# Optimization experiments

Hardware: AMD Instinct MI355X
Metric: run time of the kernel (lower is better)

The kernel has to match this reference:

```python
import jax, jax.numpy as jnp
import numpy as np
import math

B, T, C, H, L, V = 8, 511, 1024, 16, 8, 128  # T = block_size - 1
D = C // H
FF = 4 * C


def setup_inputs() -> dict:
    key = jax.random.key(0)
    ks = jax.random.split(key, 12)
    std = 0.02
    n = lambda k, s: (jax.random.normal(k, s, dtype=jnp.float32) * std)
    idx = jax.random.randint(ks[0], (B, T), 0, V)
    idx = jnp.where(idx == 2, 3, idx)  # avoid pad token so logits[idx!=2] keeps all rows
    return {
        "idx": idx,
        "tok_emb": n(ks[1], (V, C)),
        "pos_emb": n(ks[2], (T, C)),
        "ln1_w": jnp.ones((L, C)), "ln1_b": jnp.zeros((L, C)),
        "Wq": n(ks[3], (L, C, C)), "bq": jnp.zeros((L, C)),
        "Wk": n(ks[4], (L, C, C)), "bk": jnp.zeros((L, C)),
        "Wv": n(ks[5], (L, C, C)), "bv": jnp.zeros((L, C)),
        "Wp": n(ks[6], (L, C, C)), "bp": jnp.zeros((L, C)),
        "ln2_w": jnp.ones((L, C)), "ln2_b": jnp.zeros((L, C)),
        "W1": n(ks[7], (L, C, FF)), "b1": jnp.zeros((L, FF)),
        "W2": n(ks[8], (L, FF, C)), "b2": jnp.zeros((L, C)),
        "lnf_w": jnp.ones((C,)), "lnf_b": jnp.zeros((C,)),
        "head_w": n(ks[9], (V, C)),
    }


def _ln(x, w, b):
    m = x.mean(-1, keepdims=True)
    v = ((x - m) ** 2).mean(-1, keepdims=True)
    return (x - m) * jax.lax.rsqrt(v + 1e-5) * w + b


def reference(idx, tok_emb, pos_emb, ln1_w, ln1_b, Wq, bq, Wk, bk, Wv, bv, Wp, bp,
              ln2_w, ln2_b, W1, b1, W2, b2, lnf_w, lnf_b, head_w):
    x = tok_emb[idx] + pos_emb[None, :, :]                      # [B,T,C]
    mask = jnp.tril(jnp.ones((T, T), dtype=bool))
    scale = 1.0 / math.sqrt(D)

    def block(x, p):
        h = _ln(x, p["ln1_w"], p["ln1_b"])
        q = (h @ p["Wq"] + p["bq"]).reshape(B, T, H, D).transpose(0, 2, 1, 3)
        k = (h @ p["Wk"] + p["bk"]).reshape(B, T, H, D).transpose(0, 2, 1, 3)
        v = (h @ p["Wv"] + p["bv"]).reshape(B, T, H, D).transpose(0, 2, 1, 3)
        att = jnp.einsum('bhqd,bhkd->bhqk', q, k) * scale       # [B,H,T,T]
        att = jnp.where(mask, att, -jnp.inf)
        att = jax.nn.softmax(att, axis=-1)
        y = jnp.einsum('bhqk,bhkd->bhqd', att, v)
        y = y.transpose(0, 2, 1, 3).reshape(B, T, C)
        x = x + y @ p["Wp"] + p["bp"]
        h = _ln(x, p["ln2_w"], p["ln2_b"])
        h = jax.nn.gelu(h @ p["W1"] + p["b1"], approximate=False)
        x = x + h @ p["W2"] + p["b2"]
        return x, None

    stacked = dict(ln1_w=ln1_w, ln1_b=ln1_b, Wq=Wq, bq=bq, Wk=Wk, bk=bk, Wv=Wv, bv=bv,
                   Wp=Wp, bp=bp, ln2_w=ln2_w, ln2_b=ln2_b, W1=W1, b1=b1, W2=W2, b2=b2)
    x, _ = jax.lax.scan(block, x, stacked)
    x = _ln(x, lnf_w, lnf_b)
    logits = x @ head_w.T                                       # [B,T,V]
    # logits[idx != 2] with no 2-tokens present == all rows flattened
    return logits.reshape(B * T, V)
```

## Files before the change

### kernel.cpp

```cpp
#include <hip/hip_runtime.h>
#include <hip/hip_bf16.h>

typedef unsigned short u16;
typedef unsigned int   u32;
typedef __attribute__((ext_vector_type(8))) __bf16 bf16x8;
typedef __attribute__((ext_vector_type(4))) float  f32x4;

static constexpr int NB  = 8;
static constexpr int TT  = 511;
static constexpr int CC  = 1024;
static constexpr int HH  = 16;
static constexpr int LL  = 8;
static constexpr int VV  = 128;
static constexpr int FF_ = 4096;
static constexpr int MV  = NB * TT;
static constexpr int MP  = 4096;
static constexpr int TP  = 512;

#define DEVI static __device__ __forceinline__

DEVI u16 f2bf(float f) {
  u32 u = __builtin_bit_cast(u32, f);
  u = (u + 0x7fffu + ((u >> 16) & 1u)) >> 16;
  return (u16)u;
}

DEVI void gload16(const void* g, void* lds) {
  auto gp = (const __attribute__((address_space(1))) u32*)(uintptr_t)g;
  auto lp = (__attribute__((address_space(3))) u32*)(uintptr_t)lds;
  __builtin_amdgcn_global_load_lds(gp, lp, 16, 0, 0);
}

__global__ __launch_bounds__(256) void k_transpose(const float* __restrict__ in,
                                                   u16* __restrict__ out, int K, int N,
                                                   size_t is, size_t os) {
  in  += (size_t)blockIdx.z * is;
  out += (size_t)blockIdx.z * os;
  __shared__ u16 tile[64][66];
  int nb = blockIdx.x * 64, kb = blockIdx.y * 64;
  int t = threadIdx.x;
  int r = t >> 4, c4 = (t & 15) * 4;
#pragma unroll
  for (int i = 0; i < 4; ++i) {
    int k = r + i * 16;
    float4 v = *(const float4*)(in + (size_t)(kb + k) * N + nb + c4);
    tile[k][c4 + 0] = f2bf(v.x); tile[k][c4 + 1] = f2bf(v.y);
    tile[k][c4 + 2] = f2bf(v.z); tile[k][c4 + 3] = f2bf(v.w);
  }
  __syncthreads();
#pragma unroll
  for (int i = 0; i < 4; ++i) {
    int n = r + i * 16;
    ushort4 o;
    o.x = tile[c4 + 0][n]; o.y = tile[c4 + 1][n];
    o.z = tile[c4 + 2][n]; o.w = tile[c4 + 3][n];
    *(ushort4*)(out + (size_t)(nb + n) * K + kb + c4) = o;
  }
}

__global__ __launch_bounds__(256) void k_cast_bf16(const float* __restrict__ in,
                                                   u16* __restrict__ out, int n) {
  int i = blockIdx.x * 256 + threadIdx.x;
  if (i < n) out[i] = f2bf(in[i]);
}

__global__ __launch_bounds__(256) void k_pack_qkv_bias(const float* __restrict__ bq,
                                                       const float* __restrict__ bk,
                                                       const float* __restrict__ bv,
                                                       float* __restrict__ out) {
  int i = blockIdx.x * 256 + threadIdx.x;
  int l = i / (3 * CC), c = i % (3 * CC);
  float v = (c < CC) ? bq[l * CC + c] : (c < 2 * CC) ? bk[l * CC + c - CC] : bv[l * CC + c - 2 * CC];
  out[i] = v;
}

__global__ __launch_bounds__(256) void k_embed(const int* __restrict__ idx,
                                               const float* __restrict__ tok,
                                               const float* __restrict__ pos,
                                               float* __restrict__ x) {
  int row = blockIdx.x;
  int c4 = threadIdx.x * 4;
  if (row >= MV) {
    *(float4*)(x + (size_t)row * CC + c4) = make_float4(0.f, 0.f, 0.f, 0.f);
    return;
  }
  int t = row % TT;
  int tid = idx[row];
  float4 a = *(const float4*)(tok + (size_t)tid * CC + c4);
  float4 p = *(const float4*)(pos + (size_t)t * CC + c4);
  a.x += p.x; a.y += p.y; a.z += p.z; a.w += p.w;
  *(float4*)(x + (size_t)row * CC + c4) = a;
}

__global__ __launch_bounds__(256) void k_ln(const float* __restrict__ x,
                                            const float* __restrict__ w,
                                            const float* __restrict__ b,
                                            u16* __restrict__ out) {
  int wid = threadIdx.x >> 6, l = threadIdx.x & 63;
  int row = blockIdx.x * 4 + wid;
  const float* xr = x + (size_t)row * CC;
  float4 v[4];
  float s = 0.f, sq = 0.f;
#pragma unroll
  for (int i = 0; i < 4; ++i) {
    v[i] = *(const float4*)(xr + (i * 64 + l) * 4);
    s  += v[i].x + v[i].y + v[i].z + v[i].w;
    sq += v[i].x * v[i].x + v[i].y * v[i].y + v[i].z * v[i].z + v[i].w * v[i].w;
  }
#pragma unroll
  for (int o = 32; o; o >>= 1) { s += __shfl_xor(s, o); sq += __shfl_xor(sq, o); }
  float mean = s * (1.f / CC);
  float var  = sq * (1.f / CC) - mean * mean;
  float rs = rsqrtf(var + 1e-5f);
#pragma unroll
  for (int i = 0; i < 4; ++i) {
    int c = (i * 64 + l) * 4;
    float4 wv = *(const float4*)(w + c);
    float4 bv = *(const float4*)(b + c);
    ushort4 o4;
    o4.x = f2bf((v[i].x - mean) * rs * wv.x + bv.x);
    o4.y = f2bf((v[i].y - mean) * rs * wv.y + bv.y);
    o4.z = f2bf((v[i].z - mean) * rs * wv.z + bv.z);
    o4.w = f2bf((v[i].w - mean) * rs * wv.w + bv.w);
    *(ushort4*)(out + (size_t)row * CC + c) = o4;
  }
}

template <int BN, int EPI, int KSPLIT>
__global__ __launch_bounds__(512, 2) void k_gemm2(const u16* __restrict__ A,
                                                  const u16* __restrict__ Wt,
                                                  const float* __restrict__ bias,
                                                  float* __restrict__ outf,
                                                  u16* __restrict__ outb,
                                                  int N, int K, int gridN, int Mv) {
  constexpr int WN  = BN / 64;
  constexpr int GLB = BN / 64;
  constexpr int GL  = 4 + GLB;
  constexpr int ATILE = 256 * 64;
  __shared__ u16 lds[2][ATILE + BN * 64];

  int t = threadIdx.x, l = t & 63, wid = t >> 6;
  int wr = wid >> 2, wc = wid & 3;
  int lr = l & 15, lk16 = (l >> 4) * 16;

  int nwg = gridDim.x, wg = blockIdx.x;
  int q = nwg >> 3, r = nwg & 7;
  int xcd = wg & 7, loc = wg >> 3;
  int swz = (xcd < r ? xcd * (q + 1) : r * (q + 1) + (xcd - r) * q) + loc;
  int mblk = swz / (gridN * KSPLIT);
  int rest = swz - mblk * (gridN * KSPLIT);
  int nblk = rest / KSPLIT;
  int kz   = rest - nblk * KSPLIT;
  int mb = mblk * 256, nb = nblk * BN;
  int Ksub = K / KSPLIT;
  int NT = Ksub >> 6;
  const u16* Ab = A  + (size_t)mb * K + (size_t)kz * Ksub;
  const u16* Bb = Wt + (size_t)nb * K + (size_t)kz * Ksub;

  int srow8 = t >> 3;
  int skb   = (t & 7) * 16;

  auto stage = [&](int kt, int b) {
    const u16* As = Ab + kt * 64;
#pragma unroll
    for (int j = 0; j < 4; ++j) {
      int row = j * 64 + srow8;
      int kb  = skb ^ ((row & 7) << 4);
      gload16(As + (size_t)row * K + (kb >> 1), &lds[b][j * 4096 + wid * 512]);
    }
    const u16* Bs = Bb + kt * 64;
#pragma unroll
    for (int j = 0; j < GLB; ++j) {
      int row = j * 64 + srow8;
      int kb  = skb ^ ((row & 7) << 4);
      gload16(Bs + (size_t)row * K + (kb >> 1), &lds[b][ATILE + j * 4096 + wid * 512]);
    }
  };

  f32x4 acc[8][WN] = {};

  auto tile = [&](int b) {
    const char* LA = (const char*)&lds[b][0];
    const char* LB = (const char*)&lds[b][ATILE];
    bf16x8 bf[2][WN];
#pragma unroll
    for (int ks = 0; ks < 2; ++ks)
#pragma unroll
      for (int n = 0; n < WN; ++n) {
        int rr = wc * (WN * 16) + n * 16 + lr;
        int kb = (ks * 64 + lk16) ^ ((rr & 7) << 4);
        bf[ks][n] = *(const bf16x8*)(LB + rr * 128 + kb);
      }
#pragma unroll
    for (int half = 0; half < 2; ++half) {
      bf16x8 af[2][4];
#pragma unroll
      for (int ks = 0; ks < 2; ++ks)
#pragma unroll
        for (int m = 0; m < 4; ++m) {
          int rr = wr * 128 + (half * 64) + m * 16 + lr;
          int kb = (ks * 64 + lk16) ^ ((rr & 7) << 4);
          af[ks][m] = *(const bf16x8*)(LA + rr * 128 + kb);
        }
      __builtin_amdgcn_s_setprio(1);
#pragma unroll
      for (int ks = 0; ks < 2; ++ks)
#pragma unroll
        for (int m = 0; m < 4; ++m)
#pragma unroll
          for (int n = 0; n < WN; ++n)
            acc[half * 4 + m][n] = __builtin_amdgcn_mfma_f32_16x16x32_bf16(
                af[ks][m], bf[ks][n], acc[half * 4 + m][n], 0, 0, 0);
      __builtin_amdgcn_s_setprio(0);
    }
  };

  stage(0, 0);
  stage(1, 1);
  asm volatile("s_waitcnt vmcnt(%0)" :: "n"(GL) : "memory");
  __builtin_amdgcn_s_barrier();
  __builtin_amdgcn_sched_barrier(0);

  for (int kt = 0; kt < NT; kt += 2) {
#pragma unroll
    for (int sub = 0; sub < 2; ++sub) {
      tile(sub);
      asm volatile("s_waitcnt lgkmcnt(0)" ::: "memory");
      __builtin_amdgcn_s_barrier();
      __builtin_amdgcn_sched_barrier(0);
      if (kt + 2 + sub < NT) {
        stage(kt + 2 + sub, sub);
        asm volatile("s_waitcnt vmcnt(%0)" :: "n"(GL) : "memory");
      } else {
        asm volatile("s_waitcnt vmcnt(0)" ::: "memory");
      }
      __builtin_amdgcn_s_barrier();
      __builtin_amdgcn_sched_barrier(0);
    }
  }

  int r0 = (l >> 4) * 4;
#pragma unroll
  for (int m = 0; m < 8; ++m) {
    int gr = mb + wr * 128 + m * 16 + r0;
#pragma unroll
    for (int n = 0; n < WN; ++n) {
      int gc = nb + wc * (WN * 16) + n * 16 + lr;
      float bv = bias[gc];
#pragma unroll
      for (int rr = 0; rr < 4; ++rr) {
        int grr = gr + rr;
        float v = acc[m][n][rr] + bv;
        size_t o = (size_t)grr * N + gc;
        if constexpr (EPI == 1) {
          outb[o] = f2bf(v);
        } else {
          float g = 0.5f * v * (1.0f + erff(v * 0.70710678f));
          outb[o] = f2bf(g);
        }
      }
    }
  }
}

template <int EPI>
__global__ __launch_bounds__(256, 2) void k_gemm3(const u16* __restrict__ A,
                                                  const u16* __restrict__ Wt,
                                                  const float* __restrict__ bias,
                                                  float* __restrict__ outf,
                                                  const float* __restrict__ resid,
                                                  int N, int K, int gridN, int Mv) {
  constexpr int BTILE = 16384;
  __shared__ u16 lds[2][128 * 64 * 2];

  int t = threadIdx.x, l = t & 63, wid = t >> 6;
  int wr = wid >> 1, wc = wid & 1;
  int lr = l & 15, lk16 = (l >> 4) * 16;

  int nwg = gridDim.x, wg = blockIdx.x;
  int q = nwg >> 3, r = nwg & 7;
  int xcd = wg & 7, loc = wg >> 3;
  int swz = (xcd < r ? xcd * (q + 1) : r * (q + 1) + (xcd - r) * q) + loc;
  int mblk = swz / gridN;
  int nblk = swz - mblk * gridN;
  int mb = mblk * 128, nb = nblk * 128;
  int NT = K >> 6;
  const u16* Ab = A  + (size_t)mb * K;
  const u16* Bb = Wt + (size_t)nb * K;

  int srow = t >> 3;
  int skb  = (t & 7) * 16;

  auto stage = [&](int kt, int b) {
    const u16* As = Ab + kt * 64;
    char* LD = (char*)&lds[b][0];
#pragma unroll
    for (int j = 0; j < 4; ++j) {
      int row = j * 32 + srow;
      int kb  = skb ^ ((row & 7) << 4);
      gload16(As + (size_t)row * K + (kb >> 1), LD + j * 4096 + t * 16);
    }
    const u16* Bs = Bb + kt * 64;
#pragma unroll
    for (int j = 0; j < 4; ++j) {
      int row = j * 32 + srow;
      int kb  = skb ^ ((row & 7) << 4);
      gload16(Bs + (size_t)row * K + (kb >> 1), LD + BTILE + j * 4096 + t * 16);
    }
  };

  f32x4 acc[4][4] = {};

  auto tile = [&](int b) {
    const char* LA = (const char*)&lds[b][0];
    const char* LB = LA + BTILE;
    bf16x8 bfr[2][4], afr[2][4];
#pragma unroll
    for (int ks = 0; ks < 2; ++ks)
#pragma unroll
      for (int n = 0; n < 4; ++n) {
        int rr = wc * 64 + n * 16 + lr;
        int kb = (ks * 64 + lk16) ^ ((rr & 7) << 4);
        bfr[ks][n] = *(const bf16x8*)(LB + rr * 128 + kb);
      }
#pragma unroll
    for (int ks = 0; ks < 2; ++ks)
#pragma unroll
      for (int m = 0; m < 4; ++m) {
        int rr = wr * 64 + m * 16 + lr;
        int kb = (ks * 64 + lk16) ^ ((rr & 7) << 4);
        afr[ks][m] = *(const bf16x8*)(LA + rr * 128 + kb);
      }
    __builtin_amdgcn_s_setprio(1);
#pragma unroll
    for (int ks = 0; ks < 2; ++ks)
#pragma unroll
      for (int m = 0; m < 4; ++m)
#pragma unroll
        for (int n = 0; n < 4; ++n)
          acc[m][n] = __builtin_amdgcn_mfma_f32_16x16x32_bf16(
              afr[ks][m], bfr[ks][n], acc[m][n], 0, 0, 0);
    __builtin_amdgcn_s_setprio(0);
  };

  stage(0, 0);
  stage(1, 1);
  asm volatile("s_waitcnt vmcnt(8)" ::: "memory");
  __builtin_amdgcn_s_barrier();
  __builtin_amdgcn_sched_barrier(0);

  for (int kt = 0; kt < NT; kt += 2) {
#pragma unroll
    for (int sub = 0; sub < 2; ++sub) {
      tile(sub);
      asm volatile("s_waitcnt lgkmcnt(0)" ::: "memory");
      __builtin_amdgcn_s_barrier();
      __builtin_amdgcn_sched_barrier(0);
      if (kt + 2 + sub < NT) {
        stage(kt + 2 + sub, sub);
        asm volatile("s_waitcnt vmcnt(8)" ::: "memory");
      } else {
        asm volatile("s_waitcnt vmcnt(0)" ::: "memory");
      }
      __builtin_amdgcn_s_barrier();
      __builtin_amdgcn_sched_barrier(0);
    }
  }

  int r0 = (l >> 4) * 4;
#pragma unroll
  for (int m = 0; m < 4; ++m) {
    int gr = mb + wr * 64 + m * 16 + r0;
#pragma unroll
    for (int n = 0; n < 4; ++n) {
      int gc = nb + wc * 64 + n * 16 + lr;
      float bv = 0.f;
      if constexpr (EPI == 0) bv = bias[gc];
#pragma unroll
      for (int rr = 0; rr < 4; ++rr) {
        int grr = gr + rr;
        float v = acc[m][n][rr] + bv;
        size_t o = (size_t)grr * N + gc;
        if constexpr (EPI == 0) {
          outf[o] = v + resid[o];
        } else {
          if (grr < Mv) outf[o] = v;
        }
      }
    }
  }
}

__global__ __launch_bounds__(256) void k_vtrans(const u16* __restrict__ qkv,
                                                u16* __restrict__ vt) {
  __shared__ u16 tile[64][66];
  int bh = blockIdx.y;
  int b = bh >> 4, h = bh & 15;
  int t0 = blockIdx.x * 64;
  int t = threadIdx.x;
  int r = t >> 4, c4 = (t & 15) * 4;
#pragma unroll
  for (int i = 0; i < 4; ++i) {
    int tt = r + i * 16;
    int trow = t0 + tt;
    int srow = b * TT + (trow < TT ? trow : TT - 1);
    ushort4 v = *(const ushort4*)(qkv + (size_t)srow * 3072 + 2048 + h * 64 + c4);
    tile[tt][c4 + 0] = v.x; tile[tt][c4 + 1] = v.y;
    tile[tt][c4 + 2] = v.z; tile[tt][c4 + 3] = v.w;
  }
  __syncthreads();
#pragma unroll
  for (int i = 0; i < 4; ++i) {
    int d = r + i * 16;
    ushort4 o;
    o.x = (t0 + c4 + 0 < TT) ? tile[c4 + 0][d] : (u16)0;
    o.y = (t0 + c4 + 1 < TT) ? tile[c4 + 1][d] : (u16)0;
    o.z = (t0 + c4 + 2 < TT) ? tile[c4 + 2][d] : (u16)0;
    o.w = (t0 + c4 + 3 < TT) ? tile[c4 + 3][d] : (u16)0;
    *(ushort4*)(vt + ((size_t)bh * 64 + d) * TP + t0 + c4) = o;
  }
}

__global__ __launch_bounds__(512, 2) void k_attn2(const u16* __restrict__ qkv,
                                                  const u16* __restrict__ vt,
                                                  u16* __restrict__ y) {
  __shared__ u16 Kb[2][64 * 64];
  __shared__ u16 Vb[2][64 * 64];
  __shared__ u16 Pb[8][16 * 64];
  int t = threadIdx.x, l = t & 63, w = t >> 6;

  int nwg = gridDim.x, wg = blockIdx.x;
  int swz = (wg & 7) * (nwg >> 3) + (wg >> 3);
  int bh = swz >> 2, qt = swz & 3;
  int b = bh >> 4, h = bh & 15;
  int q0 = qt * 128;
  int lr = l & 15, lg = l >> 4, lk8 = lg * 8;

  const float ISC = 0.125f;

  bf16x8 Qa[2];
  {
    int qs = q0 + w * 16 + lr;
    const u16* qp = qkv + (size_t)(b * TT + (qs < TT ? qs : TT - 1)) * 3072 + h * 64;
    Qa[0] = *(const bf16x8*)(qp + lk8);
    Qa[1] = *(const bf16x8*)(qp + 32 + lk8);
  }

  int NT = (q0 + 128) >> 6;

  int srow = w * 8 + (l >> 3);
  int sb16 = (l & 7) * 16;
  int bcol = sb16 ^ ((srow & 7) << 4);
  const u16* Ksrc = qkv + 1024 + h * 64;
  const char* Vsrc = (const char*)(vt + ((size_t)bh * 64 + srow) * TP);

  auto stage = [&](int kt, int buf) {
    int kv0 = kt * 64;
    int kvr = kv0 + srow;
    int krow = b * TT + (kvr < TT ? kvr : TT - 1);
    gload16((const char*)(Ksrc + (size_t)krow * 3072) + bcol, (char*)&Kb[buf][0] + t * 16);
    gload16(Vsrc + kv0 * 2 + bcol, (char*)&Vb[buf][0] + t * 16);
  };

  f32x4 O[4] = {};
  float m_[4], s_[4];
#pragma unroll
  for (int r = 0; r < 4; ++r) { m_[r] = -1e30f; s_[r] = 0.f; }

  stage(0, 0);
  for (int kt = 0; kt < NT; ++kt) {
    int buf = kt & 1;
    if (kt + 1 < NT) {
      stage(kt + 1, buf ^ 1);
      asm volatile("s_waitcnt vmcnt(2)" ::: "memory");
    } else {
      asm volatile("s_waitcnt vmcnt(0)" ::: "memory");
    }
    __builtin_amdgcn_s_barrier();

    int kv0 = kt * 64;
    f32x4 S[4];
    const char* LK = (const char*)&Kb[buf][0];
#pragma unroll
    for (int j = 0; j < 4; ++j) {
      f32x4 a = {};
#pragma unroll
      for (int ks = 0; ks < 2; ++ks) {
        int row = j * 16 + lr;
        int kb = ((ks * 32 + lk8) * 2) ^ ((row & 7) << 4);
        bf16x8 kf = *(const bf16x8*)(LK + row * 128 + kb);
        a = __builtin_amdgcn_mfma_f32_16x16x32_bf16(Qa[ks], kf, a, 0, 0, 0);
      }
      S[j] = a;
    }
    int qbase = q0 + w * 16 + lg * 4;
#pragma unroll
    for (int j = 0; j < 4; ++j) {
      int kv = kv0 + j * 16 + lr;
#pragma unroll
      for (int r = 0; r < 4; ++r) {
        bool valid = (kv <= qbase + r) && (kv < TT);
        S[j][r] = valid ? S[j][r] : -1e30f;
      }
    }
    float mx[4];
#pragma unroll
    for (int r = 0; r < 4; ++r)
      mx[r] = fmaxf(fmaxf(S[0][r], S[1][r]), fmaxf(S[2][r], S[3][r]));
#pragma unroll
    for (int r = 0; r < 4; ++r) {
      mx[r] = fmaxf(mx[r], __shfl_xor(mx[r], 1));
      mx[r] = fmaxf(mx[r], __shfl_xor(mx[r], 2));
      mx[r] = fmaxf(mx[r], __shfl_xor(mx[r], 4));
      mx[r] = fmaxf(mx[r], __shfl_xor(mx[r], 8));
    }
    float sc[4];
#pragma unroll
    for (int r = 0; r < 4; ++r) {
      float mn = fmaxf(m_[r], mx[r]);
      sc[r] = __expf((m_[r] - mn) * ISC);
      m_[r] = mn;
      s_[r] *= sc[r];
    }
#pragma unroll
    for (int j = 0; j < 4; ++j)
#pragma unroll
      for (int r = 0; r < 4; ++r) O[j][r] *= sc[r];
    float rs[4] = {0.f, 0.f, 0.f, 0.f};
    char* LP = (char*)&Pb[w][0];
#pragma unroll
    for (int j = 0; j < 4; ++j) {
#pragma unroll
      for (int r = 0; r < 4; ++r) {
        float p = __expf((S[j][r] - m_[r]) * ISC);
        rs[r] += p;
        int row = lg * 4 + r;
        int addr = (row * 128 + (j * 16 + lr) * 2) ^ ((row & 7) << 4);
        *(u16*)(LP + addr) = f2bf(p);
      }
    }
#pragma unroll
    for (int r = 0; r < 4; ++r) {
      rs[r] += __shfl_xor(rs[r], 1);
      rs[r] += __shfl_xor(rs[r], 2);
      rs[r] += __shfl_xor(rs[r], 4);
      rs[r] += __shfl_xor(rs[r], 8);
      s_[r] += rs[r];
    }
    bf16x8 Pa[2];
#pragma unroll
    for (int ks = 0; ks < 2; ++ks) {
      int addr = (lr * 128 + (ks * 32 + lk8) * 2) ^ ((lr & 7) << 4);
      Pa[ks] = *(const bf16x8*)(LP + addr);
    }
    const char* LV = (const char*)&Vb[buf][0];
#pragma unroll
    for (int j = 0; j < 4; ++j) {
#pragma unroll
      for (int ks = 0; ks < 2; ++ks) {
        int row = j * 16 + lr;
        int kb = ((ks * 32 + lk8) * 2) ^ ((row & 7) << 4);
        bf16x8 vf = *(const bf16x8*)(LV + row * 128 + kb);
        O[j] = __builtin_amdgcn_mfma_f32_16x16x32_bf16(Pa[ks], vf, O[j], 0, 0, 0);
      }
    }
    asm volatile("s_waitcnt lgkmcnt(0)" ::: "memory");
    __builtin_amdgcn_s_barrier();
  }

  int qs0 = q0 + w * 16 + lg * 4;
#pragma unroll
  for (int r = 0; r < 4; ++r) {
    float inv = 1.0f / s_[r];
    int qs = qs0 + r;
    if (qs < TT) {
      u16* yp = y + (size_t)(b * TT + qs) * CC + h * 64;
#pragma unroll
      for (int j = 0; j < 4; ++j)
        yp[j * 16 + lr] = f2bf(O[j][r] * inv);
    }
  }
}

extern "C" void kernel_launch(void* const* d_in, const int* in_sizes, int n_in,
                              void* d_out, int out_size, void* d_ws, size_t ws_size,
                              hipStream_t stream) {
  (void)in_sizes; (void)n_in; (void)out_size; (void)ws_size;
  const int*   idx  = (const int*)  d_in[0];
  const float* tok  = (const float*)d_in[1];
  const float* pos  = (const float*)d_in[2];
  const float* ln1w = (const float*)d_in[3];
  const float* ln1b = (const float*)d_in[4];
  const float* Wq   = (const float*)d_in[5];
  const float* bq   = (const float*)d_in[6];
  const float* Wk   = (const float*)d_in[7];
  const float* bk   = (const float*)d_in[8];
  const float* Wv   = (const float*)d_in[9];
  const float* bv   = (const float*)d_in[10];
  const float* Wp   = (const float*)d_in[11];
  const float* bp   = (const float*)d_in[12];
  const float* ln2w = (const float*)d_in[13];
  const float* ln2b = (const float*)d_in[14];
  const float* W1   = (const float*)d_in[15];
  const float* b1   = (const float*)d_in[16];
  const float* W2   = (const float*)d_in[17];
  const float* b2   = (const float*)d_in[18];
  const float* lnfw = (const float*)d_in[19];
  const float* lnfb = (const float*)d_in[20];
  const float* headw= (const float*)d_in[21];
  float* out = (float*)d_out;

  char* p = (char*)d_ws;
  auto alloc = [&](size_t bytes) { char* r = p; p += (bytes + 255) & ~(size_t)255; return r; };
  u16*   wqkv_t = (u16*)  alloc((size_t)LL * 3 * CC * CC * 2);
  u16*   wp_t   = (u16*)  alloc((size_t)LL * CC * CC * 2);
  u16*   w1_t   = (u16*)  alloc((size_t)LL * FF_ * CC * 2);
  u16*   w2_t   = (u16*)  alloc((size_t)LL * CC * FF_ * 2);
  u16*   headb  = (u16*)  alloc((size_t)VV * CC * 2);
  float* bqkv   = (float*)alloc((size_t)LL * 3 * CC * 4);
  float* x      = (float*)alloc((size_t)MP * CC * 4);
  u16*   hbuf   = (u16*)  alloc((size_t)MP * CC * 2);
  u16*   qkv    = (u16*)  alloc((size_t)MP * 3 * CC * 2);
  u16*   vt     = (u16*)  alloc((size_t)NB * HH * 64 * TP * 2);
  u16*   ybuf   = (u16*)  alloc((size_t)MP * CC * 2);
  u16*   ffb    = (u16*)  alloc((size_t)MP * FF_ * 2);

  k_transpose<<<dim3(16, 16, LL), 256, 0, stream>>>(Wq, wqkv_t,                      CC, CC, (size_t)CC * CC, (size_t)3 * CC * CC);
  k_transpose<<<dim3(16, 16, LL), 256, 0, stream>>>(Wk, wqkv_t + (size_t)CC * CC,    CC, CC, (size_t)CC * CC, (size_t)3 * CC * CC);
  k_transpose<<<dim3(16, 16, LL), 256, 0, stream>>>(Wv, wqkv_t + (size_t)2 * CC * CC,CC, CC, (size_t)CC * CC, (size_t)3 * CC * CC);
  k_transpose<<<dim3(16, 16, LL), 256, 0, stream>>>(Wp, wp_t,                        CC, CC, (size_t)CC * CC, (size_t)CC * CC);
  k_transpose<<<dim3(64, 16, LL), 256, 0, stream>>>(W1, w1_t,                        CC, FF_, (size_t)CC * FF_, (size_t)FF_ * CC);
  k_transpose<<<dim3(16, 64, LL), 256, 0, stream>>>(W2, w2_t,                        FF_, CC, (size_t)FF_ * CC, (size_t)CC * FF_);
  k_cast_bf16<<<(VV * CC + 255) / 256, 256, 0, stream>>>(headw, headb, VV * CC);
  k_pack_qkv_bias<<<(LL * 3 * CC) / 256, 256, 0, stream>>>(bq, bk, bv, bqkv);

  k_embed<<<MP, 256, 0, stream>>>(idx, tok, pos, x);

  for (int l = 0; l < LL; ++l) {
    k_ln<<<MP / 4, 256, 0, stream>>>(x, ln1w + (size_t)l * CC, ln1b + (size_t)l * CC, hbuf);
    k_gemm2<256, 1, 1><<<12 * 16, 512, 0, stream>>>(hbuf, wqkv_t + (size_t)l * 3 * CC * CC,
                                                    bqkv + (size_t)l * 3 * CC, nullptr, qkv, 3 * CC, CC, 12, MP);
    k_vtrans<<<dim3(8, NB * HH), 256, 0, stream>>>(qkv, vt);
    k_attn2<<<NB * HH * 4, 512, 0, stream>>>(qkv, vt, ybuf);
    k_gemm3<0><<<32 * 8, 256, 0, stream>>>(ybuf, wp_t + (size_t)l * CC * CC,
                                           bp + (size_t)l * CC, x, x, CC, CC, 8, MP);
    k_ln<<<MP / 4, 256, 0, stream>>>(x, ln2w + (size_t)l * CC, ln2b + (size_t)l * CC, hbuf);
    k_gemm2<256, 2, 1><<<16 * 16, 512, 0, stream>>>(hbuf, w1_t + (size_t)l * FF_ * CC,
                                                    b1 + (size_t)l * FF_, nullptr, ffb, FF_, CC, 16, MP);
    k_gemm3<0><<<32 * 8, 256, 0, stream>>>(ffb, w2_t + (size_t)l * CC * FF_,
                                           b2 + (size_t)l * CC, x, x, CC, FF_, 8, MP);
  }

  k_ln<<<MP / 4, 256, 0, stream>>>(x, lnfw, lnfb, hbuf);
  k_gemm3<3><<<32 * 1, 256, 0, stream>>>(hbuf, headb, nullptr, out, nullptr, VV, CC, 1, MV);
}
```

Baseline: 1.716 ms.

## Replace 256x256 GEMM with finer-grained interleaved load/MFMA pipeline kernel

Replaces the k_gemm2 kernel used for the QKV and FC1 projections with k_gemm4. The new kernel splits each 64-deep K tile into four half-tiles (two A halves, two B halves) and issues their global-to-LDS loads between the four MFMA quarter-steps of each tile, so memory traffic overlaps compute more evenly. The warp tiling also changes: each warp now covers 64-row strips in both 128-row halves. It adds a barrier per quarter-step and drops the launch bound to one workgroup per CU, which risks lower occupancy and extra synchronisation cost.

Measured after the change: 1.695 ms. No clear change (-1.2%).

```diff
diff --git a/kernel.cpp b/kernel.cpp
--- a/kernel.cpp
+++ b/kernel.cpp
@@ -126,132 +126,131 @@
   }
 }
 
-template <int BN, int EPI, int KSPLIT>
-__global__ __launch_bounds__(512, 2) void k_gemm2(const u16* __restrict__ A,
+template <int EPI>
+__global__ __launch_bounds__(512, 1) void k_gemm4(const u16* __restrict__ A,
                                                   const u16* __restrict__ Wt,
                                                   const float* __restrict__ bias,
-                                                  float* __restrict__ outf,
                                                   u16* __restrict__ outb,
-                                                  int N, int K, int gridN, int Mv) {
-  constexpr int WN  = BN / 64;
-  constexpr int GLB = BN / 64;
-  constexpr int GL  = 4 + GLB;
-  constexpr int ATILE = 256 * 64;
-  __shared__ u16 lds[2][ATILE + BN * 64];
-
+                                                  int N, int K, int gridN) {
+  __shared__ char lds[2][4][16384];
   int t = threadIdx.x, l = t & 63, wid = t >> 6;
   int wr = wid >> 2, wc = wid & 3;
   int lr = l & 15, lk16 = (l >> 4) * 16;
 
   int nwg = gridDim.x, wg = blockIdx.x;
-  int q = nwg >> 3, r = nwg & 7;
+  int qq = nwg >> 3, r8 = nwg & 7;
   int xcd = wg & 7, loc = wg >> 3;
-  int swz = (xcd < r ? xcd * (q + 1) : r * (q + 1) + (xcd - r) * q) + loc;
-  int mblk = swz / (gridN * KSPLIT);
-  int rest = swz - mblk * (gridN * KSPLIT);
-  int nblk = rest / KSPLIT;
-  int kz   = rest - nblk * KSPLIT;
-  int mb = mblk * 256, nb = nblk * BN;
-  int Ksub = K / KSPLIT;
-  int NT = Ksub >> 6;
-  const u16* Ab = A  + (size_t)mb * K + (size_t)kz * Ksub;
-  const u16* Bb = Wt + (size_t)nb * K + (size_t)kz * Ksub;
-
-  int srow8 = t >> 3;
-  int skb   = (t & 7) * 16;
-
-  auto stage = [&](int kt, int b) {
-    const u16* As = Ab + kt * 64;
-#pragma unroll
-    for (int j = 0; j < 4; ++j) {
-      int row = j * 64 + srow8;
-      int kb  = skb ^ ((row & 7) << 4);
-      gload16(As + (size_t)row * K + (kb >> 1), &lds[b][j * 4096 + wid * 512]);
-    }
-    const u16* Bs = Bb + kt * 64;
-#pragma unroll
-    for (int j = 0; j < GLB; ++j) {
-      int row = j * 64 + srow8;
-      int kb  = skb ^ ((row & 7) << 4);
-      gload16(Bs + (size_t)row * K + (kb >> 1), &lds[b][ATILE + j * 4096 + wid * 512]);
+  int swz = (xcd < r8 ? xcd * (qq + 1) : r8 * (qq + 1) + (xcd - r8) * qq) + loc;
+  int mblk = swz / gridN, nblk = swz - mblk * gridN;
+  int mb = mblk * 256, nb = nblk * 256;
+  int NT = K >> 6;
+  const u16* Ab = A  + (size_t)mb * K;
+  const u16* Bb = Wt + (size_t)nb * K;
+
+  int srow = t >> 3, skb = (t & 7) * 16;
+
+  auto stageH = [&](int kt, int ht) {
+    int b = kt & 1;
+    const u16* src = (ht < 2) ? Ab : Bb;
+    int rowbase = (ht & 1) << 7;
+    char* dst = &lds[b][ht][0];
+    const u16* s0 = src + (size_t)rowbase * K + kt * 64;
+#pragma unroll
+    for (int j = 0; j < 2; ++j) {
+      int row = j * 64 + srow;
+      int kb = skb ^ ((row & 7) << 4);
+      gload16(s0 + (size_t)row * K + (kb >> 1), dst + j * 8192 + t * 16);
     }
   };
 
-  f32x4 acc[8][WN] = {};
-
-  auto tile = [&](int b) {
-    const char* LA = (const char*)&lds[b][0];
-    const char* LB = (const char*)&lds[b][ATILE];
-    bf16x8 bf[2][WN];
-#pragma unroll
-    for (int ks = 0; ks < 2; ++ks)
-#pragma unroll
-      for (int n = 0; n < WN; ++n) {
-        int rr = wc * (WN * 16) + n * 16 + lr;
-        int kb = (ks * 64 + lk16) ^ ((rr & 7) << 4);
-        bf[ks][n] = *(const bf16x8*)(LB + rr * 128 + kb);
-      }
-#pragma unroll
-    for (int half = 0; half < 2; ++half) {
-      bf16x8 af[2][4];
-#pragma unroll
-      for (int ks = 0; ks < 2; ++ks)
-#pragma unroll
-        for (int m = 0; m < 4; ++m) {
-          int rr = wr * 128 + (half * 64) + m * 16 + lr;
-          int kb = (ks * 64 + lk16) ^ ((rr & 7) << 4);
-          af[ks][m] = *(const bf16x8*)(LA + rr * 128 + kb);
-        }
-      __builtin_amdgcn_s_setprio(1);
-#pragma unroll
-      for (int ks = 0; ks < 2; ++ks)
-#pragma unroll
-        for (int m = 0; m < 4; ++m)
-#pragma unroll
-          for (int n = 0; n < WN; ++n)
-            acc[half * 4 + m][n] = __builtin_amdgcn_mfma_f32_16x16x32_bf16(
-                af[ks][m], bf[ks][n], acc[half * 4 + m][n], 0, 0, 0);
-      __builtin_amdgcn_s_setprio(0);
-    }
-  };
-
-  stage(0, 0);
-  stage(1, 1);
-  asm volatile("s_waitcnt vmcnt(%0)" :: "n"(GL) : "memory");
+  f32x4 acc[8][4] = {};
+
+  stageH(0, 0); stageH(0, 1); stageH(0, 2); stageH(0, 3);
+  stageH(1, 2); stageH(1, 0); stageH(1, 3);
+  asm volatile("s_waitcnt vmcnt(6)" ::: "memory");
   __builtin_amdgcn_s_barrier();
   __builtin_amdgcn_sched_barrier(0);
 
   for (int kt = 0; kt < NT; kt += 2) {
-#pragma unroll
-    for (int sub = 0; sub < 2; ++sub) {
-      tile(sub);
-      asm volatile("s_waitcnt lgkmcnt(0)" ::: "memory");
-      __builtin_amdgcn_s_barrier();
-      __builtin_amdgcn_sched_barrier(0);
-      if (kt + 2 + sub < NT) {
-        stage(kt + 2 + sub, sub);
-        asm volatile("s_waitcnt vmcnt(%0)" :: "n"(GL) : "memory");
-      } else {
-        asm volatile("s_waitcnt vmcnt(0)" ::: "memory");
-      }
-      __builtin_amdgcn_s_barrier();
-      __builtin_amdgcn_sched_barrier(0);
+    bool s2 = (kt + 2) < NT, s3 = (kt + 3) < NT;
+#pragma unroll
+    for (int half = 0; half < 2; ++half) {
+      int buf = half;
+      bf16x8 Bf[2][4];
+#pragma unroll
+      for (int q = 0; q < 4; ++q) {
+        bf16x8 Af[2][2];
+        if (q == 0) {
+#pragma unroll
+          for (int ks = 0; ks < 2; ++ks)
+#pragma unroll
+            for (int nf = 0; nf < 4; ++nf) {
+              int grow = ((wc & 1) << 6) + nf * 16 + lr;
+              int kb = (ks * 64 + lk16) ^ ((grow & 7) << 4);
+              Bf[ks][nf] = *(const bf16x8*)(&lds[buf][2 + (wc >> 1)][0] + grow * 128 + kb);
+            }
+        }
+#pragma unroll
+        for (int ks = 0; ks < 2; ++ks)
+#pragma unroll
+          for (int dm = 0; dm < 2; ++dm) {
+            int mf = q * 2 + dm;
+            int grow = wr * 64 + (mf & 3) * 16 + lr;
+            int kb = (ks * 64 + lk16) ^ ((grow & 7) << 4);
+            Af[ks][dm] = *(const bf16x8*)(&lds[buf][mf >> 2][0] + grow * 128 + kb);
+          }
+        if (half == 0) {
+          if (q == 0)      stageH(kt + 1, 1);
+          else if (q == 1) { if (s2) stageH(kt + 2, 2); }
+          else if (q == 2) { if (s2) stageH(kt + 2, 0); }
+          else             { if (s2) stageH(kt + 2, 3); }
+        } else {
+          if (q == 0)      { if (s2) stageH(kt + 2, 1); }
+          else if (q == 1) { if (s3) stageH(kt + 3, 2); }
+          else if (q == 2) { if (s3) stageH(kt + 3, 0); }
+          else             { if (s3) stageH(kt + 3, 3); }
+        }
+        __builtin_amdgcn_sched_barrier(0);
+        __builtin_amdgcn_s_barrier();
+        asm volatile("s_waitcnt lgkmcnt(0)" ::: "memory");
+        __builtin_amdgcn_sched_barrier(0);
+        __builtin_amdgcn_s_setprio(1);
+#pragma unroll
+        for (int ks = 0; ks < 2; ++ks)
+#pragma unroll
+          for (int dm = 0; dm < 2; ++dm)
+#pragma unroll
+            for (int nf = 0; nf < 4; ++nf)
+              acc[q * 2 + dm][nf] = __builtin_amdgcn_mfma_f32_16x16x32_bf16(
+                  Af[ks][dm], Bf[ks][nf], acc[q * 2 + dm][nf], 0, 0, 0);
+        __builtin_amdgcn_s_setprio(0);
+        if (q == 3) {
+          if (half == 0) {
+            if (s2) asm volatile("s_waitcnt vmcnt(6)" ::: "memory");
+            else    asm volatile("s_waitcnt vmcnt(0)" ::: "memory");
+          } else if (s2) {
+            if (s3) asm volatile("s_waitcnt vmcnt(6)" ::: "memory");
+            else    asm volatile("s_waitcnt vmcnt(0)" ::: "memory");
+          }
+        }
+        __builtin_amdgcn_sched_barrier(0);
+        __builtin_amdgcn_s_barrier();
+      }
     }
   }
 
   int r0 = (l >> 4) * 4;
 #pragma unroll
-  for (int m = 0; m < 8; ++m) {
-    int gr = mb + wr * 128 + m * 16 + r0;
-#pragma unroll
-    for (int n = 0; n < WN; ++n) {
-      int gc = nb + wc * (WN * 16) + n * 16 + lr;
+  for (int mf = 0; mf < 8; ++mf) {
+    int gr = mb + ((mf >> 2) << 7) + wr * 64 + (mf & 3) * 16 + r0;
+#pragma unroll
+    for (int nf = 0; nf < 4; ++nf) {
+      int gc = nb + wc * 64 + nf * 16 + lr;
       float bv = bias[gc];
 #pragma unroll
       for (int rr = 0; rr < 4; ++rr) {
-        int grr = gr + rr;
-        float v = acc[m][n][rr] + bv;
-        size_t o = (size_t)grr * N + gc;
+        float v = acc[mf][nf][rr] + bv;
+        size_t o = (size_t)(gr + rr) * N + gc;
         if constexpr (EPI == 1) {
           outb[o] = f2bf(v);
         } else {
@@ -638,15 +637,15 @@
 
   for (int l = 0; l < LL; ++l) {
     k_ln<<<MP / 4, 256, 0, stream>>>(x, ln1w + (size_t)l * CC, ln1b + (size_t)l * CC, hbuf);
-    k_gemm2<256, 1, 1><<<12 * 16, 512, 0, stream>>>(hbuf, wqkv_t + (size_t)l * 3 * CC * CC,
-                                                    bqkv + (size_t)l * 3 * CC, nullptr, qkv, 3 * CC, CC, 12, MP);
+    k_gemm4<1><<<12 * 16, 512, 0, stream>>>(hbuf, wqkv_t + (size_t)l * 3 * CC * CC,
+                                            bqkv + (size_t)l * 3 * CC, qkv, 3 * CC, CC, 12);
     k_vtrans<<<dim3(8, NB * HH), 256, 0, stream>>>(qkv, vt);
     k_attn2<<<NB * HH * 4, 512, 0, stream>>>(qkv, vt, ybuf);
     k_gemm3<0><<<32 * 8, 256, 0, stream>>>(ybuf, wp_t + (size_t)l * CC * CC,
                                            bp + (size_t)l * CC, x, x, CC, CC, 8, MP);
     k_ln<<<MP / 4, 256, 0, stream>>>(x, ln2w + (size_t)l * CC, ln2b + (size_t)l * CC, hbuf);
-    k_gemm2<256, 2, 1><<<16 * 16, 512, 0, stream>>>(hbuf, w1_t + (size_t)l * FF_ * CC,
-                                                    b1 + (size_t)l * FF_, nullptr, ffb, FF_, CC, 16, MP);
+    k_gemm4<2><<<16 * 16, 512, 0, stream>>>(hbuf, w1_t + (size_t)l * FF_ * CC,
+                                            b1 + (size_t)l * FF_, ffb, FF_, CC, 16);
     k_gemm3<0><<<32 * 8, 256, 0, stream>>>(ffb, w2_t + (size_t)l * CC * FF_,
                                            b2 + (size_t)l * CC, x, x, CC, FF_, 8, MP);
   }
```
